# Optimization experiments

Hardware: AMD Instinct MI355X
Metric: run time of the kernel (lower is better)

## Reference

```python
import jax, jax.numpy as jnp
import numpy as np

K = 1024  # num_embeddings
D = 256   # embedding_dim
COMMIT = 0.25

def setup_inputs() -> dict:
    key = jax.random.key(0)
    k1, k2 = jax.random.split(key)
    z = jax.random.normal(k1, (32, 256, 32, 32), dtype=jnp.float32)
    # matches nn.Embedding init uniform_(-1/K, 1/K)
    emb = jax.random.uniform(k2, (K, D), dtype=jnp.float32, minval=-1.0 / K, maxval=1.0 / K)
    return {"z": z, "emb": emb}

def reference(z, emb):
    B, C, H, W = z.shape
    zp = jnp.transpose(z, (0, 2, 3, 1))            # (B,H,W,C)
    z_flat = zp.reshape(-1, C)                      # (N,D)
    # squared euclidean distances (N,K)
    d = (jnp.sum(z_flat * z_flat, axis=1, keepdims=True)
         + jnp.sum(emb * emb, axis=1)
         - 2.0 * z_flat @ emb.T)
    idx = jnp.argmin(d, axis=1)                     # (N,)
    quantized_flat = emb[idx]                       # gather == one-hot @ emb
    quantized = quantized_flat.reshape(zp.shape)    # (B,H,W,C)
    e_latent_loss = jnp.mean((jax.lax.stop_gradient(quantized) - zp) ** 2)
    q_latent_loss = jnp.mean((quantized - jax.lax.stop_gradient(zp)) ** 2)
    loss = q_latent_loss + COMMIT * e_latent_loss
    # straight-through estimator
    quantized_st = zp + jax.lax.stop_gradient(quantized - zp)
    # perplexity: avg one-hot probs == normalized counts
    N = z_flat.shape[0]
    counts = jnp.zeros((K,), dtype=jnp.float32).at[idx].add(1.0)
    avg_probs = counts / N
    perplexity = jnp.exp(-jnp.sum(avg_probs * jnp.log(avg_probs + 1e-10)))
    out = jnp.transpose(quantized_st, (0, 3, 1, 2))  # (B,C,H,W)
    return (out, loss, perplexity)
```

## Files before the change

kernel.cpp:

```cpp
#include <hip/hip_runtime.h>
#include <math.h>

#define KC 1024
#define DD 256
#define NROWS 32768
#define NELEM 8388608

typedef _Float16 f16;
typedef __attribute__((ext_vector_type(8))) _Float16 f16x8;
typedef __attribute__((ext_vector_type(16))) float f32x16;

#define KEY_SCALE 2097152.0f
#define KEY_INV   (1.0f / 2097152.0f)

__global__ void vq_prep_kernel(const float* __restrict__ emb, f16* __restrict__ emb_h,
                               float* __restrict__ c_sq, int* __restrict__ counts,
                               float* __restrict__ loss_acc, unsigned* __restrict__ done) {
    const int tid = threadIdx.x;
    const int gt = blockIdx.x * 256 + tid;
    if (gt < KC) counts[gt] = 0;
    if (gt == 0) { *loss_acc = 0.0f; *done = 0u; }
    {
        int k = blockIdx.x * 4 + (tid >> 6);
        int lane = tid & 63;
        float4 v = *(const float4*)(emb + (size_t)k * DD + lane * 4);
        float s = v.x * v.x + v.y * v.y + v.z * v.z + v.w * v.w;
        #pragma unroll
        for (int off = 32; off > 0; off >>= 1) s += __shfl_down(s, off);
        if (lane == 0) c_sq[k] = s;
    }
    if (gt < 32768) {
        int code = gt & 1023;
        int kg = gt >> 10;
        const float* p = emb + (size_t)code * DD + kg * 8;
        float4 v0 = *(const float4*)p;
        float4 v1 = *(const float4*)(p + 4);
        f16x8 h;
        h[0] = (f16)v0.x; h[1] = (f16)v0.y; h[2] = (f16)v0.z; h[3] = (f16)v0.w;
        h[4] = (f16)v1.x; h[5] = (f16)v1.y; h[6] = (f16)v1.z; h[7] = (f16)v1.w;
        *(f16x8*)(emb_h + (size_t)gt * 8) = h;
    }
}

__global__ __launch_bounds__(512, 4)
void vq_main_kernel(const float* __restrict__ z, const float* __restrict__ emb,
                    const f16* __restrict__ emb_h, const float* __restrict__ c_sq,
                    int* __restrict__ counts, float* __restrict__ loss_acc,
                    unsigned* __restrict__ done, float* __restrict__ out,
                    float* __restrict__ out_tail) {
    __shared__ __align__(16) char smem_raw[66560];
    __shared__ int   bl_key[8][64];
    __shared__ float zsq_part[8][64];
    __shared__ int   idx_s[64];
    __shared__ float wsum[8];
    __shared__ int   last_flag;

    f16* z_s = (f16*)smem_raw;
    float* Qh = (float*)smem_raw;

    const int tid = threadIdx.x;
    const int n0 = blockIdx.x * 64;
    const int b = n0 >> 10;
    const int hw0 = n0 & 1023;

    {
        const int r = tid & 63;
        const int kq = tid >> 6;
        const float* zp = z + (size_t)b * (DD * 1024) + hw0 + r;
        float sq = 0.f;
        #pragma unroll
        for (int it = 0; it < 4; ++it) {
            int kg = kq * 4 + it;
            f16x8 hv;
            #pragma unroll
            for (int j = 0; j < 8; ++j) {
                float v = zp[(size_t)(kg * 8 + j) * 1024];
                sq += v * v;
                hv[j] = (f16)v;
            }
            *(f16x8*)&z_s[(kg * 64 + r) * 8] = hv;
        }
        zsq_part[kq][r] = sq;
    }
    __syncthreads();

    const int m = tid & 31;
    const int h = (tid >> 5) & 1;
    const int w = tid >> 6;

    int bk[32];
    #pragma unroll
    for (int s = 0; s < 32; ++s) bk[s] = 0x7FFFFFFF;

    for (int c = 0; c < 4; ++c) {
        const int cb = w * 128 + c * 32;
        const int code = cb + m;
        const f16* ebp = emb_h + (size_t)h * 8192 + (size_t)code * 8;

        f32x16 acc0, acc1;
        #pragma unroll
        for (int i = 0; i < 16; ++i) { acc0[i] = 0.f; acc1[i] = 0.f; }

        #pragma unroll 4
        for (int ks = 0; ks < 16; ++ks) {
            const f16* za = z_s + (2 * ks + h) * 512 + m * 8;
            f16x8 a0 = *(const f16x8*)(za);
            f16x8 a1 = *(const f16x8*)(za + 256);
            f16x8 b0 = *(const f16x8*)(ebp + (size_t)ks * 16384);
            acc0 = __builtin_amdgcn_mfma_f32_32x32x16_f16(a0, b0, acc0, 0, 0, 0);
            acc1 = __builtin_amdgcn_mfma_f32_32x32x16_f16(a1, b0, acc1, 0, 0, 0);
        }

        const float cs = c_sq[code];
        #pragma unroll
        for (int reg = 0; reg < 16; ++reg) {
            float s0 = fmaf(-2.f, acc0[reg], cs);
            float s1 = fmaf(-2.f, acc1[reg], cs);
            int k0 = (int)(s0 * KEY_SCALE) * 1024 + code;
            int k1 = (int)(s1 * KEY_SCALE) * 1024 + code;
            bk[reg] = min(bk[reg], k0);
            bk[16 + reg] = min(bk[16 + reg], k1);
        }
    }

    #pragma unroll
    for (int s = 0; s < 32; ++s) {
        int k = bk[s];
        #pragma unroll
        for (int d = 16; d >= 1; d >>= 1) k = min(k, __shfl_xor(k, d));
        bk[s] = k;
    }
    if (m == 0) {
        #pragma unroll
        for (int s = 0; s < 32; ++s) {
            int rt = s >> 4, reg = s & 15;
            int row = rt * 32 + (reg & 3) + 8 * (reg >> 2) + 4 * h;
            bl_key[w][row] = bk[s];
        }
    }
    __syncthreads();

    if (tid < 64) {
        int k = bl_key[0][tid];
        #pragma unroll
        for (int w2 = 1; w2 < 8; ++w2) k = min(k, bl_key[w2][tid]);
        int i = k & 1023;
        idx_s[tid] = i;
        atomicAdd(&counts[i], 1);
        float zq = 0.f;
        #pragma unroll
        for (int p = 0; p < 8; ++p) zq += zsq_part[p][tid];
        float lr = (float)(k >> 10) * KEY_INV + zq;
        #pragma unroll
        for (int off = 32; off > 0; off >>= 1) lr += __shfl_down(lr, off);
        if (tid == 0) atomicAdd(loss_acc, lr);
    }
    __syncthreads();

    {
        int r = tid & 63;
        int part = tid >> 6;
        const float* ep = emb + (size_t)idx_s[r] * DD + part * 32;
        float* qrow = Qh + r * 260 + part * 32;
        #pragma unroll
        for (int g = 0; g < 8; ++g)
            *(float4*)(qrow + g * 4) = *(const float4*)(ep + g * 4);
    }
    __syncthreads();

    {
        int r = tid & 63;
        const float* qr = Qh + r * 260;
        const size_t base = (size_t)b * (DD * 1024) + hw0 + r;
        #pragma unroll
        for (int g = 0; g < 8; ++g) {
            int c0 = w * 32 + g * 4;
            float4 v = *(const float4*)(qr + c0);
            out[base + (size_t)c0 * 1024] = v.x;
            out[base + (size_t)(c0 + 1) * 1024] = v.y;
            out[base + (size_t)(c0 + 2) * 1024] = v.z;
            out[base + (size_t)(c0 + 3) * 1024] = v.w;
        }
    }

    __syncthreads();
    if (tid == 0) {
        __threadfence();
        last_flag = (atomicAdd(done, 1u) == 511u) ? 1 : 0;
    }
    __syncthreads();
    if (last_flag) {
        __threadfence();
        float s = 0.f;
        for (int k = tid; k < KC; k += 512) {
            int cnt = atomicAdd(&counts[k], 0);
            float p = (float)cnt * (1.0f / (float)NROWS);
            s += p * logf(p + 1e-10f);
        }
        #pragma unroll
        for (int off = 32; off > 0; off >>= 1) s += __shfl_down(s, off);
        if ((tid & 63) == 0) wsum[w] = s;
        __syncthreads();
        if (tid == 0) {
            float ent = 0.f;
            #pragma unroll
            for (int p = 0; p < 8; ++p) ent += wsum[p];
            float ls = atomicAdd(loss_acc, 0.0f);
            out_tail[0] = 1.25f * ls * (1.0f / (float)NELEM);
            out_tail[1] = expf(-ent);
        }
    }
}

extern "C" void kernel_launch(void* const* d_in, const int* in_sizes, int n_in,
                              void* d_out, int out_size, void* d_ws, size_t ws_size,
                              hipStream_t stream) {
    const float* z = (const float*)d_in[0];
    const float* emb = (const float*)d_in[1];
    float* out = (float*)d_out;

    char* wsb = (char*)d_ws;
    f16* emb_h = (f16*)wsb;
    float* c_sq = (float*)(wsb + 524288);
    int* counts = (int*)(wsb + 528384);
    float* loss_acc = (float*)(wsb + 532480);
    unsigned* done = (unsigned*)(wsb + 532484);

    hipLaunchKernelGGL(vq_prep_kernel, dim3(256), dim3(256), 0, stream,
                       emb, emb_h, c_sq, counts, loss_acc, done);
    hipLaunchKernelGGL(vq_main_kernel, dim3(512), dim3(512), 0, stream,
                       z, emb, emb_h, c_sq, counts, loss_acc, done, out, out + NELEM);
}
```

Before: 132.9 us.

## Halve rows per block to 32, doubling grid and spreading loss atomics

Each main-kernel block now handles 32 rows instead of 64. That halves shared memory and MFMA accumulators per block, doubles the grid to 1024 blocks, and raises the launch-bounds occupancy hint. The loss accumulation is spread across 64 slots to reduce contention on one atomic, and the count/loss atomics are moved after the output writes. The intent is more blocks in flight across CUs to hide latency. In exchange, each block reloads all of emb_h for only half as many rows, doubling codebook traffic relative to useful MFMA work.

```diff
diff --git a/kernel.cpp b/kernel.cpp
--- a/kernel.cpp
+++ b/kernel.cpp
@@ -15,11 +15,12 @@
 
 __global__ void vq_prep_kernel(const float* __restrict__ emb, f16* __restrict__ emb_h,
                                float* __restrict__ c_sq, int* __restrict__ counts,
-                               float* __restrict__ loss_acc, unsigned* __restrict__ done) {
+                               float* __restrict__ loss64, unsigned* __restrict__ done) {
     const int tid = threadIdx.x;
     const int gt = blockIdx.x * 256 + tid;
     if (gt < KC) counts[gt] = 0;
-    if (gt == 0) { *loss_acc = 0.0f; *done = 0u; }
+    if (gt < 64) loss64[gt] = 0.0f;
+    if (gt == 0) *done = 0u;
     {
         int k = blockIdx.x * 4 + (tid >> 6);
         int lane = tid & 63;
@@ -35,23 +36,23 @@
         const float* p = emb + (size_t)code * DD + kg * 8;
         float4 v0 = *(const float4*)p;
         float4 v1 = *(const float4*)(p + 4);
-        f16x8 h;
-        h[0] = (f16)v0.x; h[1] = (f16)v0.y; h[2] = (f16)v0.z; h[3] = (f16)v0.w;
-        h[4] = (f16)v1.x; h[5] = (f16)v1.y; h[6] = (f16)v1.z; h[7] = (f16)v1.w;
-        *(f16x8*)(emb_h + (size_t)gt * 8) = h;
+        f16x8 hcv;
+        hcv[0] = (f16)v0.x; hcv[1] = (f16)v0.y; hcv[2] = (f16)v0.z; hcv[3] = (f16)v0.w;
+        hcv[4] = (f16)v1.x; hcv[5] = (f16)v1.y; hcv[6] = (f16)v1.z; hcv[7] = (f16)v1.w;
+        *(f16x8*)(emb_h + (size_t)gt * 8) = hcv;
     }
 }
 
-__global__ __launch_bounds__(512, 4)
+__global__ __launch_bounds__(512, 6)
 void vq_main_kernel(const float* __restrict__ z, const float* __restrict__ emb,
                     const f16* __restrict__ emb_h, const float* __restrict__ c_sq,
-                    int* __restrict__ counts, float* __restrict__ loss_acc,
+                    int* __restrict__ counts, float* __restrict__ loss64,
                     unsigned* __restrict__ done, float* __restrict__ out,
                     float* __restrict__ out_tail) {
-    __shared__ __align__(16) char smem_raw[66560];
-    __shared__ int   bl_key[8][64];
-    __shared__ float zsq_part[8][64];
-    __shared__ int   idx_s[64];
+    __shared__ __align__(16) char smem_raw[33280];
+    __shared__ int   bl_key[8][32];
+    __shared__ float zsq_part[16][32];
+    __shared__ int   idx_s[32];
     __shared__ float wsum[8];
     __shared__ int   last_flag;
 
@@ -59,18 +60,18 @@
     float* Qh = (float*)smem_raw;
 
     const int tid = threadIdx.x;
-    const int n0 = blockIdx.x * 64;
+    const int n0 = blockIdx.x * 32;
     const int b = n0 >> 10;
     const int hw0 = n0 & 1023;
 
     {
-        const int r = tid & 63;
-        const int kq = tid >> 6;
+        const int r = tid & 31;
+        const int kq = tid >> 5;
         const float* zp = z + (size_t)b * (DD * 1024) + hw0 + r;
         float sq = 0.f;
         #pragma unroll
-        for (int it = 0; it < 4; ++it) {
-            int kg = kq * 4 + it;
+        for (int it = 0; it < 2; ++it) {
+            int kg = kq * 2 + it;
             f16x8 hv;
             #pragma unroll
             for (int j = 0; j < 8; ++j) {
@@ -78,7 +79,7 @@
                 sq += v * v;
                 hv[j] = (f16)v;
             }
-            *(f16x8*)&z_s[(kg * 64 + r) * 8] = hv;
+            *(f16x8*)&z_s[(kg * 32 + r) * 8] = hv;
         }
         zsq_part[kq][r] = sq;
     }
@@ -88,43 +89,36 @@
     const int h = (tid >> 5) & 1;
     const int w = tid >> 6;
 
-    int bk[32];
+    int bk[16];
     #pragma unroll
-    for (int s = 0; s < 32; ++s) bk[s] = 0x7FFFFFFF;
+    for (int s = 0; s < 16; ++s) bk[s] = 0x7FFFFFFF;
 
     for (int c = 0; c < 4; ++c) {
-        const int cb = w * 128 + c * 32;
-        const int code = cb + m;
+        const int code = w * 128 + c * 32 + m;
         const f16* ebp = emb_h + (size_t)h * 8192 + (size_t)code * 8;
 
-        f32x16 acc0, acc1;
-        #pragma unroll
-        for (int i = 0; i < 16; ++i) { acc0[i] = 0.f; acc1[i] = 0.f; }
+        f32x16 acc;
+        #pragma unroll
+        for (int i = 0; i < 16; ++i) acc[i] = 0.f;
 
         #pragma unroll 4
         for (int ks = 0; ks < 16; ++ks) {
-            const f16* za = z_s + (2 * ks + h) * 512 + m * 8;
-            f16x8 a0 = *(const f16x8*)(za);
-            f16x8 a1 = *(const f16x8*)(za + 256);
+            f16x8 a0 = *(const f16x8*)(z_s + ((2 * ks + h) * 32 + m) * 8);
             f16x8 b0 = *(const f16x8*)(ebp + (size_t)ks * 16384);
-            acc0 = __builtin_amdgcn_mfma_f32_32x32x16_f16(a0, b0, acc0, 0, 0, 0);
-            acc1 = __builtin_amdgcn_mfma_f32_32x32x16_f16(a1, b0, acc1, 0, 0, 0);
+            acc = __builtin_amdgcn_mfma_f32_32x32x16_f16(a0, b0, acc, 0, 0, 0);
         }
 
         const float cs = c_sq[code];
         #pragma unroll
         for (int reg = 0; reg < 16; ++reg) {
-            float s0 = fmaf(-2.f, acc0[reg], cs);
-            float s1 = fmaf(-2.f, acc1[reg], cs);
+            float s0 = fmaf(-2.f, acc[reg], cs);
             int k0 = (int)(s0 * KEY_SCALE) * 1024 + code;
-            int k1 = (int)(s1 * KEY_SCALE) * 1024 + code;
             bk[reg] = min(bk[reg], k0);
-            bk[16 + reg] = min(bk[16 + reg], k1);
         }
     }
 
     #pragma unroll
-    for (int s = 0; s < 32; ++s) {
+    for (int s = 0; s < 16; ++s) {
         int k = bk[s];
         #pragma unroll
         for (int d = 16; d >= 1; d >>= 1) k = min(k, __shfl_xor(k, d));
@@ -132,49 +126,50 @@
     }
     if (m == 0) {
         #pragma unroll
-        for (int s = 0; s < 32; ++s) {
-            int rt = s >> 4, reg = s & 15;
-            int row = rt * 32 + (reg & 3) + 8 * (reg >> 2) + 4 * h;
+        for (int s = 0; s < 16; ++s) {
+            int row = (s & 3) + 8 * (s >> 2) + 4 * h;
             bl_key[w][row] = bk[s];
         }
     }
     __syncthreads();
 
-    if (tid < 64) {
+    int my_idx = 0;
+    float block_loss = 0.f;
+    if (tid < 32) {
         int k = bl_key[0][tid];
         #pragma unroll
         for (int w2 = 1; w2 < 8; ++w2) k = min(k, bl_key[w2][tid]);
-        int i = k & 1023;
-        idx_s[tid] = i;
-        atomicAdd(&counts[i], 1);
+        my_idx = k & 1023;
+        idx_s[tid] = my_idx;
         float zq = 0.f;
         #pragma unroll
-        for (int p = 0; p < 8; ++p) zq += zsq_part[p][tid];
+        for (int p = 0; p < 16; ++p) zq += zsq_part[p][tid];
         float lr = (float)(k >> 10) * KEY_INV + zq;
         #pragma unroll
-        for (int off = 32; off > 0; off >>= 1) lr += __shfl_down(lr, off);
-        if (tid == 0) atomicAdd(loss_acc, lr);
-    }
-    __syncthreads();
-
-    {
-        int r = tid & 63;
-        int part = tid >> 6;
-        const float* ep = emb + (size_t)idx_s[r] * DD + part * 32;
-        float* qrow = Qh + r * 260 + part * 32;
-        #pragma unroll
-        for (int g = 0; g < 8; ++g)
+        for (int off = 16; off > 0; off >>= 1) lr += __shfl_down(lr, off);
+        block_loss = lr;
+    }
+    __syncthreads();
+
+    {
+        int r = tid & 31;
+        int part = tid >> 5;
+        const float* ep = emb + (size_t)idx_s[r] * DD + part * 16;
+        float* qrow = Qh + r * 260 + part * 16;
+        #pragma unroll
+        for (int g = 0; g < 4; ++g)
             *(float4*)(qrow + g * 4) = *(const float4*)(ep + g * 4);
     }
     __syncthreads();
 
     {
-        int r = tid & 63;
+        int r = tid & 31;
+        int part = tid >> 5;
         const float* qr = Qh + r * 260;
         const size_t base = (size_t)b * (DD * 1024) + hw0 + r;
         #pragma unroll
-        for (int g = 0; g < 8; ++g) {
-            int c0 = w * 32 + g * 4;
+        for (int g = 0; g < 4; ++g) {
+            int c0 = part * 16 + g * 4;
             float4 v = *(const float4*)(qr + c0);
             out[base + (size_t)c0 * 1024] = v.x;
             out[base + (size_t)(c0 + 1) * 1024] = v.y;
@@ -183,10 +178,13 @@
         }
     }
 
+    if (tid < 32) atomicAdd(&counts[my_idx], 1);
+    if (tid == 0) atomicAdd(&loss64[blockIdx.x & 63], block_loss);
+
     __syncthreads();
     if (tid == 0) {
         __threadfence();
-        last_flag = (atomicAdd(done, 1u) == 511u) ? 1 : 0;
+        last_flag = (atomicAdd(done, 1u) == 1023u) ? 1 : 0;
     }
     __syncthreads();
     if (last_flag) {
@@ -194,19 +192,25 @@
         float s = 0.f;
         for (int k = tid; k < KC; k += 512) {
             int cnt = atomicAdd(&counts[k], 0);
-            float p = (float)cnt * (1.0f / (float)NROWS);
-            s += p * logf(p + 1e-10f);
+            float pr = (float)cnt * (1.0f / (float)NROWS);
+            s += pr * logf(pr + 1e-10f);
         }
         #pragma unroll
         for (int off = 32; off > 0; off >>= 1) s += __shfl_down(s, off);
-        if ((tid & 63) == 0) wsum[w] = s;
+        if ((tid & 63) == 0) wsum[tid >> 6] = s;
+        float loss_tot = 0.f;
+        if (tid < 64) {
+            float lv = atomicAdd(&loss64[tid], 0.0f);
+            #pragma unroll
+            for (int off = 32; off > 0; off >>= 1) lv += __shfl_down(lv, off);
+            loss_tot = lv;
+        }
         __syncthreads();
         if (tid == 0) {
             float ent = 0.f;
             #pragma unroll
             for (int p = 0; p < 8; ++p) ent += wsum[p];
-            float ls = atomicAdd(loss_acc, 0.0f);
-            out_tail[0] = 1.25f * ls * (1.0f / (float)NELEM);
+            out_tail[0] = 1.25f * loss_tot * (1.0f / (float)NELEM);
             out_tail[1] = expf(-ent);
         }
     }
@@ -223,11 +227,11 @@
     f16* emb_h = (f16*)wsb;
     float* c_sq = (float*)(wsb + 524288);
     int* counts = (int*)(wsb + 528384);
-    float* loss_acc = (float*)(wsb + 532480);
-    unsigned* done = (unsigned*)(wsb + 532484);
+    float* loss64 = (float*)(wsb + 532480);
+    unsigned* done = (unsigned*)(wsb + 532736);
 
     hipLaunchKernelGGL(vq_prep_kernel, dim3(256), dim3(256), 0, stream,
-                       emb, emb_h, c_sq, counts, loss_acc, done);
-    hipLaunchKernelGGL(vq_main_kernel, dim3(512), dim3(512), 0, stream,
-                       z, emb, emb_h, c_sq, counts, loss_acc, done, out, out + NELEM);
+                       emb, emb_h, c_sq, counts, loss64, done);
+    hipLaunchKernelGGL(vq_main_kernel, dim3(1024), dim3(512), 0, stream,
+                       z, emb, emb_h, c_sq, counts, loss64, done, out, out + NELEM);
 }
```

Measured after the change: 178.5 us. +34.3%, slower.
